# Kernel optimization log

Hardware: AMD Instinct MI355X
Metric: run time of the kernel (lower is better)

## Reference

```python
import jax, jax.numpy as jnp
import numpy as np

B, T, C, H = 32, 1024, 768, 64

def setup_inputs() -> dict:
    key = jax.random.key(0)
    k1, k2, k3, k4 = jax.random.split(key, 4)
    s = 0.01  # initializer_range-like scale
    return {
        "x": jax.random.normal(k1, (B, T, C), dtype=jnp.float32),
        "Wq": jax.random.normal(k2, (H, C), dtype=jnp.float32) * s,
        "Wk": jax.random.normal(k3, (H, C), dtype=jnp.float32) * s,
        "Wv": jax.random.normal(k4, (H, C), dtype=jnp.float32) * s,
    }

def reference(x, Wq, Wk, Wv):
    # Linear (no bias): y = x @ W.T  -> [B, T, H]
    q = jnp.einsum('btc,hc->bth', x, Wq)
    k = jnp.einsum('btc,hc->bth', x, Wk)
    v = jnp.einsum('btc,hc->bth', x, Wv)
    scale = k.shape[-1] ** -0.5
    att = jnp.einsum('bqh,bkh->bqk', q, k) * scale  # [B, T, T]
    t = x.shape[1]
    causal = jnp.tril(jnp.ones((t, t), dtype=bool))
    att = jnp.where(causal, att, -jnp.inf)
    att = jax.nn.softmax(att, axis=-1)
    # dropout p=0.0 -> identity
    y = jnp.einsum('bqk,bkh->bqh', att, v)  # [B, T, H]
    return y
```

## Files before the change

kernel.cpp:

```cpp
#include <hip/hip_runtime.h>
#include <hip/hip_bf16.h>
#include <stdint.h>

#define B_ 32
#define T_ 1024
#define C_ 768
#define H_ 64

typedef float f32x4 __attribute__((ext_vector_type(4)));
typedef short bf16x8 __attribute__((ext_vector_type(8)));

static __device__ __forceinline__ unsigned short f2bf(float f) {
    uint32_t u = __float_as_uint(f);
    u += 0x7fffu + ((u >> 16) & 1u);
    return (unsigned short)(u >> 16);
}

__global__ void wpack(const float* __restrict__ Wq, const float* __restrict__ Wk,
                      const float* __restrict__ Wv, unsigned short* __restrict__ Wall) {
    int i = blockIdx.x * 256 + threadIdx.x;
    int base = i * 4;
    if (base >= 192 * 768) return;
    int r = base / 768, c = base % 768;
    const float* src = (r < 64) ? (Wq + r * 768 + c)
                     : (r < 128) ? (Wk + (r - 64) * 768 + c)
                                 : (Wv + (r - 128) * 768 + c);
    float4 v = *(const float4*)src;
    ushort4 o;
    o.x = f2bf(v.x); o.y = f2bf(v.y); o.z = f2bf(v.z); o.w = f2bf(v.w);
    *(ushort4*)(Wall + base) = o;
}

#define XS 40
#define WS 40

__global__ __launch_bounds__(256)
void qkv_proj(const float* __restrict__ x, const unsigned short* __restrict__ Wall,
              unsigned short* __restrict__ qb, unsigned short* __restrict__ kb,
              unsigned short* __restrict__ vt) {
    __shared__ unsigned short x_t[64 * XS];
    __shared__ unsigned short w_t[192 * WS];
    __shared__ unsigned short tr[4][16 * 20];

    const int tid = threadIdx.x;
    const int lane = tid & 63, w = tid >> 6;
    const int rowbase = blockIdx.x * 64;
    const int mh = (w >> 1) * 2;
    const int nh = (w & 1) * 6;
    const int fr = lane & 15, fg = lane >> 4;

    f32x4 acc[2][6] = {};

    for (int ks = 0; ks < 768; ks += 32) {
        {
            int r = tid >> 3, cp = tid & 7;
            const float* xp = x + (size_t)(rowbase + r) * 768 + ks + cp * 4;
            unsigned short* dst = x_t + r * XS + cp * 4;
#pragma unroll
            for (int rr = 0; rr < 2; rr++) {
                float4 v = *(const float4*)(xp + (size_t)rr * 32 * 768);
                ushort4 o; o.x = f2bf(v.x); o.y = f2bf(v.y); o.z = f2bf(v.z); o.w = f2bf(v.w);
                *(ushort4*)(dst + rr * 32 * XS) = o;
            }
        }
        {
            int n0 = tid >> 2, cp = tid & 3;
            const unsigned short* wp = Wall + (size_t)n0 * 768 + ks + cp * 8;
            unsigned short* dst = w_t + n0 * WS + cp * 8;
#pragma unroll
            for (int p = 0; p < 3; p++) {
                int4 v = *(const int4*)(wp + (size_t)p * 64 * 768);
                *(int4*)(dst + p * 64 * WS) = v;
            }
        }
        __syncthreads();

        bf16x8 afr[2], bfr[6];
#pragma unroll
        for (int i = 0; i < 2; i++)
            afr[i] = *(const bf16x8*)(x_t + ((mh + i) * 16 + fr) * XS + fg * 8);
#pragma unroll
        for (int j = 0; j < 6; j++)
            bfr[j] = *(const bf16x8*)(w_t + ((nh + j) * 16 + fr) * WS + fg * 8);
#pragma unroll
        for (int i = 0; i < 2; i++)
#pragma unroll
            for (int j = 0; j < 6; j++)
                acc[i][j] = __builtin_amdgcn_mfma_f32_16x16x32_bf16(afr[i], bfr[j], acc[i][j], 0, 0, 0);
        __syncthreads();
    }

    const int b  = rowbase >> 10;
    const int t0 = rowbase & 1023;
    unsigned short* trp = &tr[w][0];
#pragma unroll
    for (int i = 0; i < 2; i++) {
        const int tb = t0 + (mh + i) * 16;
#pragma unroll
        for (int j = 0; j < 6; j++) {
            const int nc = (nh + j) * 16;
            if (nc < 128) {
                unsigned short* dstb = (nc < 64) ? qb : kb;
                const int col = nc & 63;
#pragma unroll
                for (int r = 0; r < 4; r++)
                    trp[(fg * 4 + r) * 20 + fr] = f2bf(acc[i][j][r]);
                int row = lane >> 2, seg = lane & 3;
                ushort4 rv = *(const ushort4*)(trp + row * 20 + seg * 4);
                *(ushort4*)(dstb + (size_t)(b * 1024 + tb + row) * 64 + col + seg * 4) = rv;
            } else {
                const int h = nc - 128 + fr;
                ushort4 o;
                o.x = f2bf(acc[i][j][0]); o.y = f2bf(acc[i][j][1]);
                o.z = f2bf(acc[i][j][2]); o.w = f2bf(acc[i][j][3]);
                *(ushort4*)(vt + (size_t)(b * 64 + h) * 1024 + tb + fg * 4) = o;
            }
        }
    }
}

__global__ __launch_bounds__(256)
void attn_mfma(const unsigned short* __restrict__ qbuf, const unsigned short* __restrict__ kbuf,
               const unsigned short* __restrict__ vtb, float* __restrict__ out) {
    __shared__ unsigned short ldsK[64 * 64];
    __shared__ unsigned short ldsV[64 * 64];
    __shared__ unsigned short ldsP[4][16 * 72];

    const int tid  = threadIdx.x;
    const int lane = tid & 63, w = tid >> 6;
    const int q16 = lane & 15, g = lane >> 4;

    const int fid = blockIdx.x;
    const int p = fid & 255, half = fid >> 8;
    const int bx = half ? (15 - (p & 15)) : (p & 15);
    const int b  = (p >> 4) + (half << 4);

    const int qrow0 = bx * 64 + w * 16;

    const unsigned short* qp = qbuf + ((size_t)(b * 1024 + qrow0 + q16) << 6);
    bf16x8 qfrag[2];
    qfrag[0] = *(const bf16x8*)(qp + (g << 3));
    qfrag[1] = *(const bf16x8*)(qp + 32 + (g << 3));

    f32x4 accO[4] = {};
    float m_run = -INFINITY, l_run = 0.f;

    for (int ci = 0; ci <= bx; ci++) {
        const int kbase = ci << 6;
#pragma unroll
        for (int rI = 0; rI < 2; rI++) {
            int t2 = tid + (rI << 8);
            int row = t2 >> 3, sl = t2 & 7;
            int4 kv = *(const int4*)(kbuf + ((size_t)(b * 1024 + kbase + row) << 6) + (sl << 3));
            *(int4*)(ldsK + (row << 6) + ((sl ^ (row & 7)) << 3)) = kv;
            int4 vv = *(const int4*)(vtb + ((size_t)(b * 64 + row) << 10) + kbase + (sl << 3));
            *(int4*)(ldsV + (row << 6) + ((sl ^ (row & 7)) << 3)) = vv;
        }
        __syncthreads();

        f32x4 accS[4] = {};
#pragma unroll
        for (int t = 0; t < 4; t++) {
            const unsigned short* kr = ldsK + (((t << 4) + q16) << 6);
#pragma unroll
            for (int s = 0; s < 2; s++) {
                bf16x8 af = *(const bf16x8*)(kr + ((((s << 2) + g) ^ (q16 & 7)) << 3));
                accS[t] = __builtin_amdgcn_mfma_f32_16x16x32_bf16(af, qfrag[s], accS[t], 0, 0, 0);
            }
        }

        const bool diag = (ci == bx);
        const int qlim = (w << 4) + q16;
        float mloc = -INFINITY;
#pragma unroll
        for (int t = 0; t < 4; t++)
#pragma unroll
            for (int r = 0; r < 4; r++) {
                float s = accS[t][r] * 0.125f;
                int kl = (t << 4) + (g << 2) + r;
                if (diag && kl > qlim) s = -INFINITY;
                accS[t][r] = s;
                mloc = fmaxf(mloc, s);
            }
        mloc = fmaxf(mloc, __shfl_xor(mloc, 16, 64));
        mloc = fmaxf(mloc, __shfl_xor(mloc, 32, 64));
        const float m_new = fmaxf(m_run, mloc);
        const float alpha = __expf(m_run - m_new);
        m_run = m_new;

        unsigned short* pl = &ldsP[w][0];
        float lloc = 0.f;
#pragma unroll
        for (int t = 0; t < 4; t++) {
            float p0 = __expf(accS[t][0] - m_new);
            float p1 = __expf(accS[t][1] - m_new);
            float p2 = __expf(accS[t][2] - m_new);
            float p3 = __expf(accS[t][3] - m_new);
            lloc += (p0 + p1) + (p2 + p3);
            uint2 pk;
            pk.x = (uint32_t)f2bf(p0) | ((uint32_t)f2bf(p1) << 16);
            pk.y = (uint32_t)f2bf(p2) | ((uint32_t)f2bf(p3) << 16);
            *(uint2*)(pl + q16 * 72 + (t << 4) + (g << 2)) = pk;
        }
        lloc += __shfl_xor(lloc, 16, 64);
        lloc += __shfl_xor(lloc, 32, 64);
        l_run = l_run * alpha + lloc;

#pragma unroll
        for (int t = 0; t < 4; t++) accO[t] *= alpha;

        bf16x8 pf0 = *(const bf16x8*)(pl + q16 * 72 + (g << 3));
        bf16x8 pf1 = *(const bf16x8*)(pl + q16 * 72 + 32 + (g << 3));
#pragma unroll
        for (int tp = 0; tp < 4; tp++) {
            const unsigned short* vr = ldsV + (((tp << 4) + q16) << 6);
            bf16x8 af0 = *(const bf16x8*)(vr + ((g ^ (q16 & 7)) << 3));
            accO[tp] = __builtin_amdgcn_mfma_f32_16x16x32_bf16(af0, pf0, accO[tp], 0, 0, 0);
            bf16x8 af1 = *(const bf16x8*)(vr + (((4 + g) ^ (q16 & 7)) << 3));
            accO[tp] = __builtin_amdgcn_mfma_f32_16x16x32_bf16(af1, pf1, accO[tp], 0, 0, 0);
        }
        __syncthreads();
    }

    const float inv = 1.0f / l_run;
    float* op = out + ((size_t)(b * 1024 + qrow0 + q16) << 6);
#pragma unroll
    for (int tp = 0; tp < 4; tp++) {
        float4 o4;
        o4.x = accO[tp][0] * inv; o4.y = accO[tp][1] * inv;
        o4.z = accO[tp][2] * inv; o4.w = accO[tp][3] * inv;
        *(float4*)(op + (tp << 4) + (g << 2)) = o4;
    }
}

extern "C" void kernel_launch(void* const* d_in, const int* in_sizes, int n_in,
                              void* d_out, int out_size, void* d_ws, size_t ws_size,
                              hipStream_t stream) {
    const float* x  = (const float*)d_in[0];
    const float* Wq = (const float*)d_in[1];
    const float* Wk = (const float*)d_in[2];
    const float* Wv = (const float*)d_in[3];

    unsigned short* Wall = (unsigned short*)d_ws;
    unsigned short* qbuf = Wall + 192 * 768;
    unsigned short* kbuf = qbuf + (size_t)B_ * T_ * H_;
    unsigned short* vtb  = kbuf + (size_t)B_ * T_ * H_;
    float* out = (float*)d_out;

    wpack<<<144, 256, 0, stream>>>(Wq, Wk, Wv, Wall);
    qkv_proj<<<512, 256, 0, stream>>>(x, Wall, qbuf, kbuf, vtb);
    attn_mfma<<<512, 256, 0, stream>>>(qbuf, kbuf, vtb, out);
}
```

Measured before the change: 194.2 us.

## Double-buffer LDS tiles with register prefetch in projection and attention kernels

Both the QKV projection and the attention kernel now hold two LDS buffers. Each iteration issues the global loads for the next K-slice or K/V chunk into registers before computing on the current buffer, then writes them to the other buffer afterwards. This removes one barrier per iteration and hides global-load latency behind the MFMA work. In exchange it doubles LDS use and raises register pressure, which could lower occupancy.

```diff
diff --git a/kernel.cpp b/kernel.cpp
--- a/kernel.cpp
+++ b/kernel.cpp
@@ -38,8 +38,8 @@
 void qkv_proj(const float* __restrict__ x, const unsigned short* __restrict__ Wall,
               unsigned short* __restrict__ qb, unsigned short* __restrict__ kb,
               unsigned short* __restrict__ vt) {
-    __shared__ unsigned short x_t[64 * XS];
-    __shared__ unsigned short w_t[192 * WS];
+    __shared__ unsigned short x_t[2][64 * XS];
+    __shared__ unsigned short w_t[2][192 * WS];
     __shared__ unsigned short tr[4][16 * 20];
 
     const int tid = threadIdx.x;
@@ -49,44 +49,55 @@
     const int nh = (w & 1) * 6;
     const int fr = lane & 15, fg = lane >> 4;
 
+    const int xrow = tid >> 3, xcp = tid & 7;
+    const int wrow = tid >> 2, wcp = tid & 3;
+
+    float4 xreg[2];
+    int4   wreg[3];
+
+#define LDQ(ks_) {                                                                \
+        const float* xp = x + (size_t)(rowbase + xrow) * 768 + (ks_) + xcp * 4;   \
+        xreg[0] = *(const float4*)xp;                                             \
+        xreg[1] = *(const float4*)(xp + 32 * 768);                                \
+        const unsigned short* wp = Wall + (size_t)wrow * 768 + (ks_) + wcp * 8;   \
+        wreg[0] = *(const int4*)(wp);                                             \
+        wreg[1] = *(const int4*)(wp + (size_t)64 * 768);                          \
+        wreg[2] = *(const int4*)(wp + (size_t)128 * 768); }
+
+#define STQ(buf_) {                                                               \
+        unsigned short* dx = &x_t[buf_][0] + xrow * XS + xcp * 4;                 \
+        _Pragma("unroll")                                                         \
+        for (int rr = 0; rr < 2; rr++) {                                          \
+            float4 v = xreg[rr]; ushort4 o;                                       \
+            o.x = f2bf(v.x); o.y = f2bf(v.y); o.z = f2bf(v.z); o.w = f2bf(v.w);   \
+            *(ushort4*)(dx + rr * 32 * XS) = o; }                                 \
+        unsigned short* dw = &w_t[buf_][0] + wrow * WS + wcp * 8;                 \
+        _Pragma("unroll")                                                         \
+        for (int p_ = 0; p_ < 3; p_++) *(int4*)(dw + p_ * 64 * WS) = wreg[p_]; }
+
     f32x4 acc[2][6] = {};
 
-    for (int ks = 0; ks < 768; ks += 32) {
-        {
-            int r = tid >> 3, cp = tid & 7;
-            const float* xp = x + (size_t)(rowbase + r) * 768 + ks + cp * 4;
-            unsigned short* dst = x_t + r * XS + cp * 4;
-#pragma unroll
-            for (int rr = 0; rr < 2; rr++) {
-                float4 v = *(const float4*)(xp + (size_t)rr * 32 * 768);
-                ushort4 o; o.x = f2bf(v.x); o.y = f2bf(v.y); o.z = f2bf(v.z); o.w = f2bf(v.w);
-                *(ushort4*)(dst + rr * 32 * XS) = o;
-            }
-        }
-        {
-            int n0 = tid >> 2, cp = tid & 3;
-            const unsigned short* wp = Wall + (size_t)n0 * 768 + ks + cp * 8;
-            unsigned short* dst = w_t + n0 * WS + cp * 8;
-#pragma unroll
-            for (int p = 0; p < 3; p++) {
-                int4 v = *(const int4*)(wp + (size_t)p * 64 * 768);
-                *(int4*)(dst + p * 64 * WS) = v;
-            }
-        }
-        __syncthreads();
+    LDQ(0); STQ(0);
+    __syncthreads();
+
+    for (int it = 0; it < 24; it++) {
+        const int cur = it & 1;
+        if (it < 23) LDQ((it + 1) * 32);
 
         bf16x8 afr[2], bfr[6];
 #pragma unroll
         for (int i = 0; i < 2; i++)
-            afr[i] = *(const bf16x8*)(x_t + ((mh + i) * 16 + fr) * XS + fg * 8);
+            afr[i] = *(const bf16x8*)(&x_t[cur][0] + ((mh + i) * 16 + fr) * XS + fg * 8);
 #pragma unroll
         for (int j = 0; j < 6; j++)
-            bfr[j] = *(const bf16x8*)(w_t + ((nh + j) * 16 + fr) * WS + fg * 8);
+            bfr[j] = *(const bf16x8*)(&w_t[cur][0] + ((nh + j) * 16 + fr) * WS + fg * 8);
 #pragma unroll
         for (int i = 0; i < 2; i++)
 #pragma unroll
             for (int j = 0; j < 6; j++)
                 acc[i][j] = __builtin_amdgcn_mfma_f32_16x16x32_bf16(afr[i], bfr[j], acc[i][j], 0, 0, 0);
+
+        if (it < 23) STQ(cur ^ 1);
         __syncthreads();
     }
 
@@ -122,8 +133,8 @@
 __global__ __launch_bounds__(256)
 void attn_mfma(const unsigned short* __restrict__ qbuf, const unsigned short* __restrict__ kbuf,
                const unsigned short* __restrict__ vtb, float* __restrict__ out) {
-    __shared__ unsigned short ldsK[64 * 64];
-    __shared__ unsigned short ldsV[64 * 64];
+    __shared__ unsigned short ldsK[2][64 * 64];
+    __shared__ unsigned short ldsV[2][64 * 64];
     __shared__ unsigned short ldsP[4][16 * 72];
 
     const int tid  = threadIdx.x;
@@ -142,26 +153,35 @@
     qfrag[0] = *(const bf16x8*)(qp + (g << 3));
     qfrag[1] = *(const bf16x8*)(qp + 32 + (g << 3));
 
+    int4 kreg[2], vreg[2];
+#define LDCH(ci_) { const int kb2 = (ci_) << 6;                                              \
+        _Pragma("unroll")                                                                    \
+        for (int rI = 0; rI < 2; rI++) { int t2 = tid + (rI << 8);                           \
+            int row = t2 >> 3, sl = t2 & 7;                                                  \
+            kreg[rI] = *(const int4*)(kbuf + ((size_t)(b * 1024 + kb2 + row) << 6) + (sl << 3)); \
+            vreg[rI] = *(const int4*)(vtb + ((size_t)(b * 64 + row) << 10) + kb2 + (sl << 3)); } }
+
+#define STCH(buf_) {                                                                         \
+        _Pragma("unroll")                                                                    \
+        for (int rI = 0; rI < 2; rI++) { int t2 = tid + (rI << 8);                           \
+            int row = t2 >> 3, sl = t2 & 7;                                                  \
+            *(int4*)(&ldsK[buf_][0] + (row << 6) + ((sl ^ (row & 7)) << 3)) = kreg[rI];      \
+            *(int4*)(&ldsV[buf_][0] + (row << 6) + ((sl ^ (row & 7)) << 3)) = vreg[rI]; } }
+
+    LDCH(0); STCH(0);
+    __syncthreads();
+
     f32x4 accO[4] = {};
     float m_run = -INFINITY, l_run = 0.f;
 
     for (int ci = 0; ci <= bx; ci++) {
-        const int kbase = ci << 6;
-#pragma unroll
-        for (int rI = 0; rI < 2; rI++) {
-            int t2 = tid + (rI << 8);
-            int row = t2 >> 3, sl = t2 & 7;
-            int4 kv = *(const int4*)(kbuf + ((size_t)(b * 1024 + kbase + row) << 6) + (sl << 3));
-            *(int4*)(ldsK + (row << 6) + ((sl ^ (row & 7)) << 3)) = kv;
-            int4 vv = *(const int4*)(vtb + ((size_t)(b * 64 + row) << 10) + kbase + (sl << 3));
-            *(int4*)(ldsV + (row << 6) + ((sl ^ (row & 7)) << 3)) = vv;
-        }
-        __syncthreads();
+        const int cur = ci & 1;
+        if (ci < bx) LDCH(ci + 1);
 
         f32x4 accS[4] = {};
 #pragma unroll
         for (int t = 0; t < 4; t++) {
-            const unsigned short* kr = ldsK + (((t << 4) + q16) << 6);
+            const unsigned short* kr = &ldsK[cur][0] + (((t << 4) + q16) << 6);
 #pragma unroll
             for (int s = 0; s < 2; s++) {
                 bf16x8 af = *(const bf16x8*)(kr + ((((s << 2) + g) ^ (q16 & 7)) << 3));
@@ -213,12 +233,14 @@
         bf16x8 pf1 = *(const bf16x8*)(pl + q16 * 72 + 32 + (g << 3));
 #pragma unroll
         for (int tp = 0; tp < 4; tp++) {
-            const unsigned short* vr = ldsV + (((tp << 4) + q16) << 6);
+            const unsigned short* vr = &ldsV[cur][0] + (((tp << 4) + q16) << 6);
             bf16x8 af0 = *(const bf16x8*)(vr + ((g ^ (q16 & 7)) << 3));
             accO[tp] = __builtin_amdgcn_mfma_f32_16x16x32_bf16(af0, pf0, accO[tp], 0, 0, 0);
             bf16x8 af1 = *(const bf16x8*)(vr + (((4 + g) ^ (q16 & 7)) << 3));
             accO[tp] = __builtin_amdgcn_mfma_f32_16x16x32_bf16(af1, pf1, accO[tp], 0, 0, 0);
         }
+
+        if (ci < bx) STCH(cur ^ 1);
         __syncthreads();
     }
 
```

Measured after the change: 232.8 us. +19.9%, slower.

## Load MFMA operands directly from global memory, dropping LDS staging and barriers

Applied to the files above, without the earlier changes.

Both the QKV projection and the attention kernel stop staging tiles in shared memory. Each wave now reads its bf16 fragments straight from global memory (x converted on the fly, W and K/V read as bf16x8), which removes the block-wide __syncthreads barriers. The projection also changes its split: each wave owns 16 rows and all 192 output columns instead of a 2x6 tile. The trade-off is that loads the block used to share, such as W in the projection and K/V in attention (read by all four waves), are now issued once per wave and rely on L1/L2 for reuse.

```diff
diff --git a/kernel.cpp b/kernel.cpp
--- a/kernel.cpp
+++ b/kernel.cpp
@@ -31,90 +31,59 @@
     *(ushort4*)(Wall + base) = o;
 }
 
-#define XS 40
-#define WS 40
-
 __global__ __launch_bounds__(256)
 void qkv_proj(const float* __restrict__ x, const unsigned short* __restrict__ Wall,
               unsigned short* __restrict__ qb, unsigned short* __restrict__ kb,
               unsigned short* __restrict__ vt) {
-    __shared__ unsigned short x_t[64 * XS];
-    __shared__ unsigned short w_t[192 * WS];
     __shared__ unsigned short tr[4][16 * 20];
 
     const int tid = threadIdx.x;
     const int lane = tid & 63, w = tid >> 6;
     const int rowbase = blockIdx.x * 64;
-    const int mh = (w >> 1) * 2;
-    const int nh = (w & 1) * 6;
     const int fr = lane & 15, fg = lane >> 4;
-
-    f32x4 acc[2][6] = {};
+    const int myrow = rowbase + w * 16 + fr;
+
+    const float*          xp  = x    + (size_t)myrow * 768 + fg * 8;
+    const unsigned short* wp0 = Wall + (size_t)fr * 768 + fg * 8;
+
+    f32x4 acc[12] = {};
 
     for (int ks = 0; ks < 768; ks += 32) {
-        {
-            int r = tid >> 3, cp = tid & 7;
-            const float* xp = x + (size_t)(rowbase + r) * 768 + ks + cp * 4;
-            unsigned short* dst = x_t + r * XS + cp * 4;
-#pragma unroll
-            for (int rr = 0; rr < 2; rr++) {
-                float4 v = *(const float4*)(xp + (size_t)rr * 32 * 768);
-                ushort4 o; o.x = f2bf(v.x); o.y = f2bf(v.y); o.z = f2bf(v.z); o.w = f2bf(v.w);
-                *(ushort4*)(dst + rr * 32 * XS) = o;
-            }
-        }
-        {
-            int n0 = tid >> 2, cp = tid & 3;
-            const unsigned short* wp = Wall + (size_t)n0 * 768 + ks + cp * 8;
-            unsigned short* dst = w_t + n0 * WS + cp * 8;
-#pragma unroll
-            for (int p = 0; p < 3; p++) {
-                int4 v = *(const int4*)(wp + (size_t)p * 64 * 768);
-                *(int4*)(dst + p * 64 * WS) = v;
-            }
-        }
-        __syncthreads();
-
-        bf16x8 afr[2], bfr[6];
-#pragma unroll
-        for (int i = 0; i < 2; i++)
-            afr[i] = *(const bf16x8*)(x_t + ((mh + i) * 16 + fr) * XS + fg * 8);
-#pragma unroll
-        for (int j = 0; j < 6; j++)
-            bfr[j] = *(const bf16x8*)(w_t + ((nh + j) * 16 + fr) * WS + fg * 8);
-#pragma unroll
-        for (int i = 0; i < 2; i++)
-#pragma unroll
-            for (int j = 0; j < 6; j++)
-                acc[i][j] = __builtin_amdgcn_mfma_f32_16x16x32_bf16(afr[i], bfr[j], acc[i][j], 0, 0, 0);
-        __syncthreads();
+        float4 xa = *(const float4*)(xp + ks);
+        float4 xb = *(const float4*)(xp + ks + 4);
+        bf16x8 af;
+        af[0] = (short)f2bf(xa.x); af[1] = (short)f2bf(xa.y);
+        af[2] = (short)f2bf(xa.z); af[3] = (short)f2bf(xa.w);
+        af[4] = (short)f2bf(xb.x); af[5] = (short)f2bf(xb.y);
+        af[6] = (short)f2bf(xb.z); af[7] = (short)f2bf(xb.w);
+#pragma unroll
+        for (int j = 0; j < 12; j++) {
+            bf16x8 bf = *(const bf16x8*)(wp0 + (size_t)j * 16 * 768 + ks);
+            acc[j] = __builtin_amdgcn_mfma_f32_16x16x32_bf16(af, bf, acc[j], 0, 0, 0);
+        }
     }
 
     const int b  = rowbase >> 10;
-    const int t0 = rowbase & 1023;
+    const int t0 = (rowbase & 1023) + w * 16;
     unsigned short* trp = &tr[w][0];
 #pragma unroll
-    for (int i = 0; i < 2; i++) {
-        const int tb = t0 + (mh + i) * 16;
-#pragma unroll
-        for (int j = 0; j < 6; j++) {
-            const int nc = (nh + j) * 16;
-            if (nc < 128) {
-                unsigned short* dstb = (nc < 64) ? qb : kb;
-                const int col = nc & 63;
-#pragma unroll
-                for (int r = 0; r < 4; r++)
-                    trp[(fg * 4 + r) * 20 + fr] = f2bf(acc[i][j][r]);
-                int row = lane >> 2, seg = lane & 3;
-                ushort4 rv = *(const ushort4*)(trp + row * 20 + seg * 4);
-                *(ushort4*)(dstb + (size_t)(b * 1024 + tb + row) * 64 + col + seg * 4) = rv;
-            } else {
-                const int h = nc - 128 + fr;
-                ushort4 o;
-                o.x = f2bf(acc[i][j][0]); o.y = f2bf(acc[i][j][1]);
-                o.z = f2bf(acc[i][j][2]); o.w = f2bf(acc[i][j][3]);
-                *(ushort4*)(vt + (size_t)(b * 64 + h) * 1024 + tb + fg * 4) = o;
-            }
+    for (int j = 0; j < 12; j++) {
+        const int nc = j * 16;
+        if (nc < 128) {
+            unsigned short* dstb = (nc < 64) ? qb : kb;
+            const int col = nc & 63;
+#pragma unroll
+            for (int r = 0; r < 4; r++)
+                trp[(fg * 4 + r) * 20 + fr] = f2bf(acc[j][r]);
+            int row = lane >> 2, seg = lane & 3;
+            ushort4 rv = *(const ushort4*)(trp + row * 20 + seg * 4);
+            *(ushort4*)(dstb + (size_t)(b * 1024 + t0 + row) * 64 + col + seg * 4) = rv;
+        } else {
+            const int h = nc - 128 + fr;
+            ushort4 o;
+            o.x = f2bf(acc[j][0]); o.y = f2bf(acc[j][1]);
+            o.z = f2bf(acc[j][2]); o.w = f2bf(acc[j][3]);
+            *(ushort4*)(vt + (size_t)(b * 64 + h) * 1024 + t0 + fg * 4) = o;
         }
     }
 }
@@ -122,8 +91,6 @@
 __global__ __launch_bounds__(256)
 void attn_mfma(const unsigned short* __restrict__ qbuf, const unsigned short* __restrict__ kbuf,
                const unsigned short* __restrict__ vtb, float* __restrict__ out) {
-    __shared__ unsigned short ldsK[64 * 64];
-    __shared__ unsigned short ldsV[64 * 64];
     __shared__ unsigned short ldsP[4][16 * 72];
 
     const int tid  = threadIdx.x;
@@ -147,24 +114,14 @@
 
     for (int ci = 0; ci <= bx; ci++) {
         const int kbase = ci << 6;
-#pragma unroll
-        for (int rI = 0; rI < 2; rI++) {
-            int t2 = tid + (rI << 8);
-            int row = t2 >> 3, sl = t2 & 7;
-            int4 kv = *(const int4*)(kbuf + ((size_t)(b * 1024 + kbase + row) << 6) + (sl << 3));
-            *(int4*)(ldsK + (row << 6) + ((sl ^ (row & 7)) << 3)) = kv;
-            int4 vv = *(const int4*)(vtb + ((size_t)(b * 64 + row) << 10) + kbase + (sl << 3));
-            *(int4*)(ldsV + (row << 6) + ((sl ^ (row & 7)) << 3)) = vv;
-        }
-        __syncthreads();
 
         f32x4 accS[4] = {};
 #pragma unroll
         for (int t = 0; t < 4; t++) {
-            const unsigned short* kr = ldsK + (((t << 4) + q16) << 6);
+            const unsigned short* kr = kbuf + ((size_t)(b * 1024 + kbase + (t << 4) + q16) << 6);
 #pragma unroll
             for (int s = 0; s < 2; s++) {
-                bf16x8 af = *(const bf16x8*)(kr + ((((s << 2) + g) ^ (q16 & 7)) << 3));
+                bf16x8 af = *(const bf16x8*)(kr + (s << 5) + (g << 3));
                 accS[t] = __builtin_amdgcn_mfma_f32_16x16x32_bf16(af, qfrag[s], accS[t], 0, 0, 0);
             }
         }
@@ -213,13 +170,12 @@
         bf16x8 pf1 = *(const bf16x8*)(pl + q16 * 72 + 32 + (g << 3));
 #pragma unroll
         for (int tp = 0; tp < 4; tp++) {
-            const unsigned short* vr = ldsV + (((tp << 4) + q16) << 6);
-            bf16x8 af0 = *(const bf16x8*)(vr + ((g ^ (q16 & 7)) << 3));
+            const unsigned short* vr = vtb + ((size_t)(b * 64 + (tp << 4) + q16) << 10) + kbase;
+            bf16x8 af0 = *(const bf16x8*)(vr + (g << 3));
             accO[tp] = __builtin_amdgcn_mfma_f32_16x16x32_bf16(af0, pf0, accO[tp], 0, 0, 0);
-            bf16x8 af1 = *(const bf16x8*)(vr + (((4 + g) ^ (q16 & 7)) << 3));
+            bf16x8 af1 = *(const bf16x8*)(vr + 32 + (g << 3));
             accO[tp] = __builtin_amdgcn_mfma_f32_16x16x32_bf16(af1, pf1, accO[tp], 0, 0, 0);
         }
-        __syncthreads();
     }
 
     const float inv = 1.0f / l_run;
```

Measured after the change: 264.5 us. 1.36x slower.
